# Optimization experiments

Measured on AMD Instinct MI355X. Metric: run time of the kernel, lower is better.

Reference implementation:

```python
import jax, jax.numpy as jnp
import numpy as np

D_MODEL = 2048
NUM_HEADS = 32
NUM_KV_HEADS = 8
D_K = D_MODEL // NUM_HEADS
B, S = 2, 2048


def setup_inputs() -> dict:
    key = jax.random.key(0)
    ks = jax.random.split(key, 6)
    sc = 1.0 / np.sqrt(D_MODEL)
    x = jax.random.normal(ks[0], (B, S, D_MODEL), dtype=jnp.float32)
    mask = jnp.tril(jnp.ones((S, S), dtype=jnp.float32))[None, None]  # [1,1,S,S]
    return {
        'x': x,
        'mask': mask,
        'Wq': jax.random.normal(ks[1], (D_MODEL, D_MODEL), jnp.float32) * sc,
        'bq': jnp.zeros((D_MODEL,), jnp.float32),
        'Wk': jax.random.normal(ks[2], (D_MODEL, NUM_KV_HEADS * D_K), jnp.float32) * sc,
        'bk': jnp.zeros((NUM_KV_HEADS * D_K,), jnp.float32),
        'Wv': jax.random.normal(ks[3], (D_MODEL, NUM_KV_HEADS * D_K), jnp.float32) * sc,
        'bv': jnp.zeros((NUM_KV_HEADS * D_K,), jnp.float32),
        'Wo': jax.random.normal(ks[4], (D_MODEL, D_MODEL), jnp.float32) * sc,
        'bo': jnp.zeros((D_MODEL,), jnp.float32),
    }


def reference(x, mask, Wq, bq, Wk, bk, Wv, bv, Wo, bo):
    b, s, _ = x.shape
    g = NUM_HEADS // NUM_KV_HEADS  # queries per kv head
    Q = (x @ Wq + bq).reshape(b, s, NUM_HEADS, D_K).transpose(0, 2, 1, 3)      # [b,h,s,dk]
    K = (x @ Wk + bk).reshape(b, s, NUM_KV_HEADS, D_K).transpose(0, 2, 1, 3)   # [b,kv,s,dk]
    V = (x @ Wv + bv).reshape(b, s, NUM_KV_HEADS, D_K).transpose(0, 2, 1, 3)
    # group queries per kv head instead of repeat_interleave on K/V
    Qg = Q.reshape(b, NUM_KV_HEADS, g, s, D_K)
    scores = jnp.einsum('bkgqd,bkld->bkgql', Qg, K) / np.sqrt(D_K)             # [b,kv,g,s,s]
    scores = jnp.where(mask[:, :, None] == 0, -1e9, scores)
    attn = jax.nn.softmax(scores, axis=-1)
    out = jnp.einsum('bkgql,bkld->bkgqd', attn, V)                              # [b,kv,g,s,dk]
    out = out.reshape(b, NUM_HEADS, s, D_K).transpose(0, 2, 1, 3).reshape(b, s, D_MODEL)
    return out @ Wo + bo
```

## Files before the change

kernel.cpp:

```cpp
#include <hip/hip_runtime.h>
#include <stdint.h>

typedef __bf16 bf16x8 __attribute__((ext_vector_type(8)));
typedef float  f32x4  __attribute__((ext_vector_type(4)));

__device__ __forceinline__ f32x4 mfma16(bf16x8 a, bf16x8 b, f32x4 c) {
    return __builtin_amdgcn_mfma_f32_16x16x32_bf16(a, b, c, 0, 0, 0);
}

__device__ __forceinline__ uint16_t f2bf(float f) {
    union { __bf16 b; uint16_t u; } cv; cv.b = (__bf16)f; return cv.u;
}

#if __has_builtin(__builtin_amdgcn_exp2f)
#define EXP2F(x) __builtin_amdgcn_exp2f(x)
#else
#define EXP2F(x) __expf((x) * 0.6931471805599453f)
#endif

typedef __attribute__((address_space(3))) void as3_void;
typedef __attribute__((address_space(1))) void as1_void;
__device__ __forceinline__ void async_ld16(const void* g, void* l) {
    __builtin_amdgcn_global_load_lds((const as1_void*)g, (as3_void*)l, 16, 0, 0);
}


__global__ void convert_bias(const float* __restrict__ in, uint16_t* __restrict__ out,
                             const float* __restrict__ bq, const float* __restrict__ bk,
                             const float* __restrict__ bv, float* __restrict__ biasq) {
    if (blockIdx.x < 8192) {
        int i = (blockIdx.x * 256 + threadIdx.x) * 4;
        float4 v = *(const float4*)(in + i);
        ushort4 o;
        o.x = f2bf(v.x); o.y = f2bf(v.y); o.z = f2bf(v.z); o.w = f2bf(v.w);
        *(ushort4*)(out + i) = o;
    } else {
        int i = (blockIdx.x - 8192) * 256 + threadIdx.x;
        if (i < 3072)
            biasq[i] = (i < 2048) ? bq[i] : (i < 2560 ? bk[i - 2048] : bv[i - 2560]);
    }
}

__global__ void transpose_w(const float* __restrict__ Wq, const float* __restrict__ Wk,
                            const float* __restrict__ Wv, const float* __restrict__ Wo,
                            uint16_t* __restrict__ wqkvT, uint16_t* __restrict__ woT) {
    __shared__ float tile[32][33];
    const int z = blockIdx.z;
    const float* in; uint16_t* out; int ldin, off;
    if (z == 0)      { in = Wq; out = wqkvT; ldin = 2048; off = 0; }
    else if (z == 1) { if (blockIdx.x >= 16) return; in = Wk; out = wqkvT; ldin = 512; off = 2048; }
    else if (z == 2) { if (blockIdx.x >= 16) return; in = Wv; out = wqkvT; ldin = 512; off = 2560; }
    else             { in = Wo; out = woT;   ldin = 2048; off = 0; }
    const int c0 = blockIdx.x << 5, r0 = blockIdx.y << 5;
    const int tx = threadIdx.x, ty = threadIdx.y;
#pragma unroll
    for (int i = 0; i < 4; ++i)
        tile[ty + i * 8][tx] = in[(size_t)(r0 + ty + i * 8) * ldin + c0 + tx];
    __syncthreads();
#pragma unroll
    for (int i = 0; i < 4; ++i)
        out[(size_t)(off + c0 + ty + i * 8) * 2048 + r0 + tx] = f2bf(tile[tx][ty + i * 8]);
}

__global__ void transpose_v(const uint16_t* __restrict__ qkv, uint16_t* __restrict__ vt) {
    __shared__ uint16_t tile[32][33];
    const int c0 = blockIdx.x << 5, r0 = blockIdx.y << 5, b = blockIdx.z;
    const int tx = threadIdx.x, ty = threadIdx.y;
#pragma unroll
    for (int i = 0; i < 4; ++i)
        tile[ty + i * 8][tx] = qkv[(size_t)(b * 2048 + r0 + ty + i * 8) * 3072 + 2560 + c0 + tx];
    __syncthreads();
    const int perm = 4 * (tx >> 3) + (((tx & 7) < 4) ? 0 : 16) + (tx & 3);
#pragma unroll
    for (int i = 0; i < 4; ++i)
        vt[(size_t)(b * 512 + c0 + ty + i * 8) * 2048 + r0 + tx] = tile[perm][ty + i * 8];
}

template <bool F32OUT>
__global__ __launch_bounds__(256, 2)
void gemm_bt(const uint16_t* __restrict__ A, const uint16_t* __restrict__ Bt,
             const float* __restrict__ bias, void* __restrict__ Cout, int N, int K) {
    __shared__ __align__(16) uint16_t As[8192];
    __shared__ __align__(16) uint16_t Bs[8192];
    const int tid = threadIdx.x;
    const int wv = tid >> 6, ln = tid & 63;
    const int quad = ln >> 4, l16 = ln & 15;
    const int row0 = blockIdx.y << 7, col0 = blockIdx.x << 7;
    const int wm = wv >> 1, wn = wv & 1;

    const uint16_t* gA[4];
    const uint16_t* gB[4];
#pragma unroll
    for (int j = 0; j < 4; ++j) {
        int p = j * 256 + tid;
        int r = p >> 3, c = (p & 7) ^ ((r ^ (r >> 3)) & 7);
        gA[j] = A + (size_t)(row0 + r) * K + (c << 3);
        gB[j] = Bt + (size_t)(col0 + r) * K + (c << 3);
    }

    int a_off[4][2], b_off[4][2];
#pragma unroll
    for (int t = 0; t < 4; ++t)
#pragma unroll
        for (int s = 0; s < 2; ++s) {
            int r = (wm << 6) + (t << 4) + l16;
            a_off[t][s] = (((r << 3) + ((4 * s + quad) ^ ((r ^ (r >> 3)) & 7))) << 3);
            r = (wn << 6) + (t << 4) + l16;
            b_off[t][s] = (((r << 3) + ((4 * s + quad) ^ ((r ^ (r >> 3)) & 7))) << 3);
        }

    f32x4 acc[4][4] = {};

    for (int k0 = 0; k0 < K; k0 += 64) {
        __syncthreads();
#pragma unroll
        for (int j = 0; j < 4; ++j) {
            async_ld16(gA[j] + k0, As + (j << 11) + (wv << 9));
            async_ld16(gB[j] + k0, Bs + (j << 11) + (wv << 9));
        }
        __syncthreads();
#pragma unroll
        for (int s = 0; s < 2; ++s) {
            bf16x8 af[4], bfr[4];
#pragma unroll
            for (int t = 0; t < 4; ++t) af[t] = *(const bf16x8*)(As + a_off[t][s]);
#pragma unroll
            for (int t = 0; t < 4; ++t) bfr[t] = *(const bf16x8*)(Bs + b_off[t][s]);
#pragma unroll
            for (int mt = 0; mt < 4; ++mt)
#pragma unroll
                for (int nt = 0; nt < 4; ++nt)
                    acc[mt][nt] = mfma16(af[mt], bfr[nt], acc[mt][nt]);
        }
    }

#pragma unroll
    for (int nt = 0; nt < 4; ++nt) {
        const int col = col0 + (wn << 6) + (nt << 4) + l16;
        const float bv = bias[col];
#pragma unroll
        for (int mt = 0; mt < 4; ++mt) {
            const int rbase = row0 + (wm << 6) + (mt << 4) + (quad << 2);
#pragma unroll
            for (int r = 0; r < 4; ++r) {
                float v = acc[mt][nt][r] + bv;
                if (F32OUT)
                    ((float*)Cout)[(size_t)(rbase + r) * N + col] = v;
                else
                    ((uint16_t*)Cout)[(size_t)(rbase + r) * N + col] = f2bf(v);
            }
        }
    }
}

__global__ __launch_bounds__(256, 2)
void attn_fwd(const uint16_t* __restrict__ QKV, const uint16_t* __restrict__ Vt,
              uint16_t* __restrict__ AO) {
    __shared__ __align__(16) uint16_t smem[16384];
    uint16_t* const Ks = smem;
    uint16_t* const Vs = smem + 8192;

    const int tid = threadIdx.x;
    const int wv = tid >> 6, ln = tid & 63;
    const int quad = ln >> 4, l16 = ln & 15;
    const int p = blockIdx.x, kvh = blockIdx.y, b = blockIdx.z;
    const int h = kvh * 4 + wv;

    const uint16_t* Kg = QKV + (size_t)(b * 2048) * 3072 + 2048 + kvh * 64;
    const uint16_t* Vg = Vt + (size_t)(b * 512 + kvh * 64) * 2048;

    const uint16_t* gK[2];
    const uint16_t* gV[2];
#pragma unroll
    for (int j = 0; j < 2; ++j) {
        int pos = j * 256 + tid;
        int r = pos >> 3, c = (pos & 7) ^ ((r ^ (r >> 3)) & 7);
        gK[j] = Kg + (size_t)r * 3072 + (c << 3);
        gV[j] = Vg + (size_t)r * 2048 + (c << 3);
    }
    const int sdst = wv << 9;

    int kf_off[4][2], vf_off[2][4];
#pragma unroll
    for (int g = 0; g < 4; ++g) {
        int r = g * 16 + l16, gs = (r ^ (r >> 3)) & 7;
#pragma unroll
        for (int kk = 0; kk < 2; ++kk)
            kf_off[g][kk] = ((r << 3) + ((kk * 4 + quad) ^ gs)) << 3;
    }
#pragma unroll
    for (int nt = 0; nt < 4; ++nt) {
        int r = nt * 16 + l16, gs = (r ^ (r >> 3)) & 7;
#pragma unroll
        for (int s = 0; s < 2; ++s)
            vf_off[s][nt] = ((r << 3) + ((s * 4 + quad) ^ gs)) << 3;
    }

#define EXP_PV(MASKED)                                                         \
    _Pragma("unroll")                                                          \
    for (int m = 0; m < 2; ++m) {                                              \
        f32x4 ev[4];                                                           \
        _Pragma("unroll")                                                      \
        for (int g = 0; g < 4; ++g) {                                          \
            f32x4 arg = sv[m][g] * 0.18033688f + (-23.0831207f);               \
            _Pragma("unroll")                                                  \
            for (int rr = 0; rr < 4; ++rr) {                                   \
                float v = EXP2F(arg[rr]);                                      \
                if (MASKED && (16 * g + 4 * quad + rr >                        \
                               32 * wr + 16 * m + l16)) v = 0.0f;              \
                ev[g][rr] = v;                                                 \
            }                                                                  \
        }                                                                      \
        f32x4 s2 = (ev[0] + ev[1]) + (ev[2] + ev[3]);                          \
        lp[m] += (s2[0] + s2[1]) + (s2[2] + s2[3]);                            \
        bf16x8 pf0, pf1;                                                       \
        _Pragma("unroll")                                                      \
        for (int rr = 0; rr < 4; ++rr) {                                       \
            pf0[rr] = (__bf16)ev[0][rr]; pf0[4 + rr] = (__bf16)ev[1][rr];      \
            pf1[rr] = (__bf16)ev[2][rr]; pf1[4 + rr] = (__bf16)ev[3][rr];      \
        }                                                                      \
        __builtin_amdgcn_s_setprio(1);                                         \
        _Pragma("unroll")                                                      \
        for (int nt = 0; nt < 4; ++nt) {                                       \
            acc[m][nt] = mfma16(vf[0][nt], pf0, acc[m][nt]);                   \
            acc[m][nt] = mfma16(vf[1][nt], pf1, acc[m][nt]);                   \
        }                                                                      \
        __builtin_amdgcn_s_setprio(0);                                         \
    }

#pragma unroll
    for (int half = 0; half < 2; ++half) {
        const int w = half ? (63 - p) : p;
        const int q0 = w << 5;
        const int nkb = (w >> 1) + 1;
        const int wr = w & 1;

        bf16x8 qf[2][2];
#pragma unroll
        for (int m = 0; m < 2; ++m)
#pragma unroll
            for (int kk = 0; kk < 2; ++kk)
                qf[m][kk] = *(const bf16x8*)(QKV +
                    (size_t)(b * 2048 + q0 + m * 16 + l16) * 3072 + h * 64 + kk * 32 + quad * 8);

        f32x4 acc[2][4] = {};
        float lp[2] = {0.0f, 0.0f};

        __syncthreads();
#pragma unroll
        for (int j = 0; j < 2; ++j) {
            async_ld16(gK[j], Ks + (j << 11) + sdst);
            async_ld16(gV[j], Vs + (j << 11) + sdst);
        }

        for (int t = 0; t < nkb; ++t) {
            const int cur = t & 1;
            __syncthreads();
            if (t + 1 < nkb) {
                const size_t ko = (size_t)((t + 1) << 6) * 3072;
                const int vo = (t + 1) << 6;
#pragma unroll
                for (int j = 0; j < 2; ++j) {
                    async_ld16(gK[j] + ko, Ks + ((cur ^ 1) << 12) + (j << 11) + sdst);
                    async_ld16(gV[j] + vo, Vs + ((cur ^ 1) << 12) + (j << 11) + sdst);
                }
            }

            bf16x8 kf[4][2], vf[2][4];
#pragma unroll
            for (int g = 0; g < 4; ++g)
#pragma unroll
                for (int kk = 0; kk < 2; ++kk)
                    kf[g][kk] = *(const bf16x8*)(Ks + (cur << 12) + kf_off[g][kk]);
#pragma unroll
            for (int s = 0; s < 2; ++s)
#pragma unroll
                for (int nt = 0; nt < 4; ++nt)
                    vf[s][nt] = *(const bf16x8*)(Vs + (cur << 12) + vf_off[s][nt]);

            f32x4 sv[2][4];
            __builtin_amdgcn_s_setprio(1);
#pragma unroll
            for (int m = 0; m < 2; ++m)
#pragma unroll
                for (int g = 0; g < 4; ++g) {
                    f32x4 z = {0.f, 0.f, 0.f, 0.f};
                    z = mfma16(kf[g][0], qf[m][0], z);
                    z = mfma16(kf[g][1], qf[m][1], z);
                    sv[m][g] = z;
                }
            __builtin_amdgcn_s_setprio(0);

            if (t < nkb - 1) {
                EXP_PV(false)
            } else {
                EXP_PV(true)
            }
        }

        float inv[2];
#pragma unroll
        for (int m = 0; m < 2; ++m) {
            float rs = lp[m];
            rs += __shfl_xor(rs, 16, 64);
            rs += __shfl_xor(rs, 32, 64);
            inv[m] = 1.0f / rs;
        }

        __syncthreads();
        uint16_t* ot = smem + wv * 2176;
#pragma unroll
        for (int m = 0; m < 2; ++m)
#pragma unroll
            for (int nt = 0; nt < 4; ++nt)
#pragma unroll
                for (int pp = 0; pp < 2; ++pp) {
                    uint32_t pk = (uint32_t)f2bf(acc[m][nt][2 * pp] * inv[m]) |
                                  ((uint32_t)f2bf(acc[m][nt][2 * pp + 1] * inv[m]) << 16);
                    *(uint32_t*)(ot + (m * 16 + l16) * 68 + nt * 16 + quad * 4 + 2 * pp) = pk;
                }
        const int orow = ln >> 1, ohalf = (ln & 1) << 5;
        uint16_t* aobase = AO + (size_t)(b * 2048 + q0 + orow) * 2048 + h * 64 + ohalf;
        const uint16_t* osrc = ot + orow * 68 + ohalf;
#pragma unroll
        for (int c4 = 0; c4 < 4; ++c4)
            *(uint4*)(aobase + c4 * 8) = *(const uint4*)(osrc + c4 * 8);
    }
#undef EXP_PV
}


extern "C" void kernel_launch(void* const* d_in, const int* in_sizes, int n_in,
                              void* d_out, int out_size, void* d_ws, size_t ws_size,
                              hipStream_t stream) {
    (void)in_sizes; (void)n_in; (void)out_size; (void)ws_size;
    const float* x  = (const float*)d_in[0];
    const float* Wq = (const float*)d_in[2];
    const float* bq = (const float*)d_in[3];
    const float* Wk = (const float*)d_in[4];
    const float* bk = (const float*)d_in[5];
    const float* Wv = (const float*)d_in[6];
    const float* bv = (const float*)d_in[7];
    const float* Wo = (const float*)d_in[8];
    const float* bo = (const float*)d_in[9];

    char* ws = (char*)d_ws;
    uint16_t* xb    = (uint16_t*)ws;
    uint16_t* wqkvT = (uint16_t*)(ws + 16777216);
    uint16_t* woT   = (uint16_t*)(ws + 16777216 + 12582912);
    float*    biasq = (float*)(ws + 16777216 + 12582912 + 8388608);
    uint16_t* qkv   = (uint16_t*)d_out;
    uint16_t* ao    = xb;
    uint16_t* vt    = wqkvT;

    dim3 tb(32, 8);
    convert_bias<<<8204, 256, 0, stream>>>(x, xb, bq, bk, bv, biasq);
    transpose_w<<<dim3(64, 64, 4), tb, 0, stream>>>(Wq, Wk, Wv, Wo, wqkvT, woT);
    gemm_bt<false><<<dim3(24, 32), 256, 0, stream>>>(xb, wqkvT, biasq, qkv, 3072, 2048);
    transpose_v<<<dim3(16, 64, 2), tb, 0, stream>>>(qkv, vt);
    attn_fwd<<<dim3(32, 8, 2), 256, 0, stream>>>(qkv, vt, ao);
    gemm_bt<true><<<dim3(16, 32), 256, 0, stream>>>(ao, woT, bo, d_out, 2048, 2048);
}
```

Baseline: 283.6 us.

## Merge prep kernels and double K/V tile window per attention barrier

Fuses the x-to-bf16 conversion and bias packing into the weight transpose kernel as an extra z-slice, removing one launch. In attention, each barrier iteration now prefetches and processes two 64-key K/V sub-tiles instead of one, with LDS doubled to 64 KB. This halves the number of __syncthreads per query block and gives loads more lead time, but the larger LDS footprint may limit occupancy against the two-blocks-per-CU launch bound.

```diff
diff --git a/kernel.cpp b/kernel.cpp
--- a/kernel.cpp
+++ b/kernel.cpp
@@ -25,34 +25,39 @@
 }
 
 
-__global__ void convert_bias(const float* __restrict__ in, uint16_t* __restrict__ out,
-                             const float* __restrict__ bq, const float* __restrict__ bk,
-                             const float* __restrict__ bv, float* __restrict__ biasq) {
-    if (blockIdx.x < 8192) {
-        int i = (blockIdx.x * 256 + threadIdx.x) * 4;
-        float4 v = *(const float4*)(in + i);
-        ushort4 o;
-        o.x = f2bf(v.x); o.y = f2bf(v.y); o.z = f2bf(v.z); o.w = f2bf(v.w);
-        *(ushort4*)(out + i) = o;
-    } else {
-        int i = (blockIdx.x - 8192) * 256 + threadIdx.x;
-        if (i < 3072)
-            biasq[i] = (i < 2048) ? bq[i] : (i < 2560 ? bk[i - 2048] : bv[i - 2560]);
-    }
-}
-
-__global__ void transpose_w(const float* __restrict__ Wq, const float* __restrict__ Wk,
-                            const float* __restrict__ Wv, const float* __restrict__ Wo,
-                            uint16_t* __restrict__ wqkvT, uint16_t* __restrict__ woT) {
+__global__ void prep_wx(const float* __restrict__ x,
+                        const float* __restrict__ Wq, const float* __restrict__ Wk,
+                        const float* __restrict__ Wv, const float* __restrict__ Wo,
+                        const float* __restrict__ bq, const float* __restrict__ bk,
+                        const float* __restrict__ bv,
+                        uint16_t* __restrict__ wqkvT, uint16_t* __restrict__ woT,
+                        uint16_t* __restrict__ xb, float* __restrict__ biasq) {
+    const int z = blockIdx.z;
+    const int tx = threadIdx.x, ty = threadIdx.y;
+    if (z == 4) {
+        const int tid = ty * 32 + tx;
+        const int linear = blockIdx.y * 64 + blockIdx.x;
+        const int i = linear * 2048 + tid * 8;
+#pragma unroll
+        for (int u = 0; u < 2; ++u) {
+            float4 v = *(const float4*)(x + i + u * 4);
+            ushort4 o;
+            o.x = f2bf(v.x); o.y = f2bf(v.y); o.z = f2bf(v.z); o.w = f2bf(v.w);
+            *(ushort4*)(xb + i + u * 4) = o;
+        }
+        if (linear < 12) {
+            int bi = linear * 256 + tid;
+            biasq[bi] = (bi < 2048) ? bq[bi] : (bi < 2560 ? bk[bi - 2048] : bv[bi - 2560]);
+        }
+        return;
+    }
     __shared__ float tile[32][33];
-    const int z = blockIdx.z;
     const float* in; uint16_t* out; int ldin, off;
     if (z == 0)      { in = Wq; out = wqkvT; ldin = 2048; off = 0; }
     else if (z == 1) { if (blockIdx.x >= 16) return; in = Wk; out = wqkvT; ldin = 512; off = 2048; }
     else if (z == 2) { if (blockIdx.x >= 16) return; in = Wv; out = wqkvT; ldin = 512; off = 2560; }
     else             { in = Wo; out = woT;   ldin = 2048; off = 0; }
     const int c0 = blockIdx.x << 5, r0 = blockIdx.y << 5;
-    const int tx = threadIdx.x, ty = threadIdx.y;
 #pragma unroll
     for (int i = 0; i < 4; ++i)
         tile[ty + i * 8][tx] = in[(size_t)(r0 + ty + i * 8) * ldin + c0 + tx];
@@ -156,9 +161,9 @@
 __global__ __launch_bounds__(256, 2)
 void attn_fwd(const uint16_t* __restrict__ QKV, const uint16_t* __restrict__ Vt,
               uint16_t* __restrict__ AO) {
-    __shared__ __align__(16) uint16_t smem[16384];
+    __shared__ __align__(16) uint16_t smem[32768];
     uint16_t* const Ks = smem;
-    uint16_t* const Vs = smem + 8192;
+    uint16_t* const Vs = smem + 16384;
 
     const int tid = threadIdx.x;
     const int wv = tid >> 6, ln = tid & 63;
@@ -228,11 +233,43 @@
         __builtin_amdgcn_s_setprio(0);                                         \
     }
 
+#define PROC(SUB)                                                              \
+    {                                                                          \
+        const uint16_t* kb = Ks + (((cur << 1) | SUB) << 12);                  \
+        const uint16_t* vb = Vs + (((cur << 1) | SUB) << 12);                  \
+        bf16x8 kf[4][2], vf[2][4];                                             \
+        _Pragma("unroll")                                                      \
+        for (int g = 0; g < 4; ++g)                                            \
+            _Pragma("unroll")                                                  \
+            for (int kk = 0; kk < 2; ++kk)                                     \
+                kf[g][kk] = *(const bf16x8*)(kb + kf_off[g][kk]);              \
+        _Pragma("unroll")                                                      \
+        for (int s = 0; s < 2; ++s)                                            \
+            _Pragma("unroll")                                                  \
+            for (int nt = 0; nt < 4; ++nt)                                     \
+                vf[s][nt] = *(const bf16x8*)(vb + vf_off[s][nt]);              \
+        f32x4 sv[2][4];                                                        \
+        __builtin_amdgcn_s_setprio(1);                                         \
+        _Pragma("unroll")                                                      \
+        for (int m = 0; m < 2; ++m)                                            \
+            _Pragma("unroll")                                                  \
+            for (int g = 0; g < 4; ++g) {                                      \
+                f32x4 z = {0.f, 0.f, 0.f, 0.f};                                \
+                z = mfma16(kf[g][0], qf[m][0], z);                             \
+                z = mfma16(kf[g][1], qf[m][1], z);                             \
+                sv[m][g] = z;                                                  \
+            }                                                                  \
+        __builtin_amdgcn_s_setprio(0);                                         \
+        if ((tw << 1) + SUB == nkb - 1) { EXP_PV(true) }                       \
+        else                            { EXP_PV(false) }                      \
+    }
+
 #pragma unroll
     for (int half = 0; half < 2; ++half) {
         const int w = half ? (63 - p) : p;
         const int q0 = w << 5;
         const int nkb = (w >> 1) + 1;
+        const int nwin = (nkb + 1) >> 1;
         const int wr = w & 1;
 
         bf16x8 qf[2][2];
@@ -248,54 +285,34 @@
 
         __syncthreads();
 #pragma unroll
-        for (int j = 0; j < 2; ++j) {
-            async_ld16(gK[j], Ks + (j << 11) + sdst);
-            async_ld16(gV[j], Vs + (j << 11) + sdst);
-        }
-
-        for (int t = 0; t < nkb; ++t) {
-            const int cur = t & 1;
+        for (int sub = 0; sub < 2; ++sub)
+#pragma unroll
+            for (int j = 0; j < 2; ++j) {
+                async_ld16(gK[j] + (size_t)(sub << 6) * 3072, Ks + (sub << 12) + (j << 11) + sdst);
+                async_ld16(gV[j] + (sub << 6),                Vs + (sub << 12) + (j << 11) + sdst);
+            }
+
+        for (int tw = 0; tw < nwin; ++tw) {
+            const int cur = tw & 1;
             __syncthreads();
-            if (t + 1 < nkb) {
-                const size_t ko = (size_t)((t + 1) << 6) * 3072;
-                const int vo = (t + 1) << 6;
-#pragma unroll
-                for (int j = 0; j < 2; ++j) {
-                    async_ld16(gK[j] + ko, Ks + ((cur ^ 1) << 12) + (j << 11) + sdst);
-                    async_ld16(gV[j] + vo, Vs + ((cur ^ 1) << 12) + (j << 11) + sdst);
+            if (tw + 1 < nwin) {
+#pragma unroll
+                for (int sub = 0; sub < 2; ++sub) {
+                    const int tn = ((tw + 1) << 1) + sub;
+                    const size_t ko = (size_t)(tn << 6) * 3072;
+                    const int vo = tn << 6;
+#pragma unroll
+                    for (int j = 0; j < 2; ++j) {
+                        async_ld16(gK[j] + ko,
+                                   Ks + ((((cur ^ 1) << 1) | sub) << 12) + (j << 11) + sdst);
+                        async_ld16(gV[j] + vo,
+                                   Vs + ((((cur ^ 1) << 1) | sub) << 12) + (j << 11) + sdst);
+                    }
                 }
             }
 
-            bf16x8 kf[4][2], vf[2][4];
-#pragma unroll
-            for (int g = 0; g < 4; ++g)
-#pragma unroll
-                for (int kk = 0; kk < 2; ++kk)
-                    kf[g][kk] = *(const bf16x8*)(Ks + (cur << 12) + kf_off[g][kk]);
-#pragma unroll
-            for (int s = 0; s < 2; ++s)
-#pragma unroll
-                for (int nt = 0; nt < 4; ++nt)
-                    vf[s][nt] = *(const bf16x8*)(Vs + (cur << 12) + vf_off[s][nt]);
-
-            f32x4 sv[2][4];
-            __builtin_amdgcn_s_setprio(1);
-#pragma unroll
-            for (int m = 0; m < 2; ++m)
-#pragma unroll
-                for (int g = 0; g < 4; ++g) {
-                    f32x4 z = {0.f, 0.f, 0.f, 0.f};
-                    z = mfma16(kf[g][0], qf[m][0], z);
-                    z = mfma16(kf[g][1], qf[m][1], z);
-                    sv[m][g] = z;
-                }
-            __builtin_amdgcn_s_setprio(0);
-
-            if (t < nkb - 1) {
-                EXP_PV(false)
-            } else {
-                EXP_PV(true)
-            }
+            PROC(0)
+            if ((tw << 1) + 1 < nkb) PROC(1)
         }
 
         float inv[2];
@@ -326,6 +343,7 @@
         for (int c4 = 0; c4 < 4; ++c4)
             *(uint4*)(aobase + c4 * 8) = *(const uint4*)(osrc + c4 * 8);
     }
+#undef PROC
 #undef EXP_PV
 }
 
@@ -354,8 +372,8 @@
     uint16_t* vt    = wqkvT;
 
     dim3 tb(32, 8);
-    convert_bias<<<8204, 256, 0, stream>>>(x, xb, bq, bk, bv, biasq);
-    transpose_w<<<dim3(64, 64, 4), tb, 0, stream>>>(Wq, Wk, Wv, Wo, wqkvT, woT);
+    prep_wx<<<dim3(64, 64, 5), tb, 0, stream>>>(x, Wq, Wk, Wv, Wo, bq, bk, bv,
+                                                wqkvT, woT, xb, biasq);
     gemm_bt<false><<<dim3(24, 32), 256, 0, stream>>>(xb, wqkvT, biasq, qkv, 3072, 2048);
     transpose_v<<<dim3(16, 64, 2), tb, 0, stream>>>(qkv, vt);
     attn_fwd<<<dim3(32, 8, 2), 256, 0, stream>>>(qkv, vt, ao);
```

Measured after the change: 285.6 us. No clear change (+0.7%).

## Process both causal query tiles concurrently in 512-thread attention blocks sharing K/V

Applied to the files above, without the earlier changes.

The attention kernel grows from 256 to 512 threads. The two query tiles each block handles (p and 63-p) now run at the same time in separate 4-wave groups instead of one after the other. Each K/V tile is loaded into LDS once and used by both groups, so the short-tile group simply idles once its own range is done. This halves K/V staging traffic and the serial second pass. The cost is idle waves in the short group, a larger LDS footprint for the output staging, and possible register pressure under launch_bounds(512,2).

```diff
diff --git a/kernel.cpp b/kernel.cpp
--- a/kernel.cpp
+++ b/kernel.cpp
@@ -153,10 +153,10 @@
     }
 }
 
-__global__ __launch_bounds__(256, 2)
+__global__ __launch_bounds__(512, 2)
 void attn_fwd(const uint16_t* __restrict__ QKV, const uint16_t* __restrict__ Vt,
               uint16_t* __restrict__ AO) {
-    __shared__ __align__(16) uint16_t smem[16384];
+    __shared__ __align__(16) uint16_t smem[17408];
     uint16_t* const Ks = smem;
     uint16_t* const Vs = smem + 8192;
 
@@ -164,19 +164,23 @@
     const int wv = tid >> 6, ln = tid & 63;
     const int quad = ln >> 4, l16 = ln & 15;
     const int p = blockIdx.x, kvh = blockIdx.y, b = blockIdx.z;
-    const int h = kvh * 4 + wv;
+    const int wg = wv >> 2;
+    const int h = kvh * 4 + (wv & 3);
+    const int w = wg ? (63 - p) : p;
+    const int q0 = w << 5;
+    const int nkbw = (w >> 1) + 1;
+    const int nkbm = ((63 - p) >> 1) + 1;
+    const int wr = w & 1;
 
     const uint16_t* Kg = QKV + (size_t)(b * 2048) * 3072 + 2048 + kvh * 64;
     const uint16_t* Vg = Vt + (size_t)(b * 512 + kvh * 64) * 2048;
 
-    const uint16_t* gK[2];
-    const uint16_t* gV[2];
-#pragma unroll
-    for (int j = 0; j < 2; ++j) {
-        int pos = j * 256 + tid;
-        int r = pos >> 3, c = (pos & 7) ^ ((r ^ (r >> 3)) & 7);
-        gK[j] = Kg + (size_t)r * 3072 + (c << 3);
-        gV[j] = Vg + (size_t)r * 2048 + (c << 3);
+    const uint16_t* gK;
+    const uint16_t* gV;
+    {
+        int r = tid >> 3, c = (tid & 7) ^ ((r ^ (r >> 3)) & 7);
+        gK = Kg + (size_t)r * 3072 + (c << 3);
+        gV = Vg + (size_t)r * 2048 + (c << 3);
     }
     const int sdst = wv << 9;
 
@@ -195,6 +199,17 @@
         for (int s = 0; s < 2; ++s)
             vf_off[s][nt] = ((r << 3) + ((s * 4 + quad) ^ gs)) << 3;
     }
+
+    bf16x8 qf[2][2];
+#pragma unroll
+    for (int m = 0; m < 2; ++m)
+#pragma unroll
+        for (int kk = 0; kk < 2; ++kk)
+            qf[m][kk] = *(const bf16x8*)(QKV +
+                (size_t)(b * 2048 + q0 + m * 16 + l16) * 3072 + h * 64 + kk * 32 + quad * 8);
+
+    f32x4 acc[2][4] = {};
+    float lp[2] = {0.0f, 0.0f};
 
 #define EXP_PV(MASKED)                                                         \
     _Pragma("unroll")                                                          \
@@ -228,44 +243,18 @@
         __builtin_amdgcn_s_setprio(0);                                         \
     }
 
-#pragma unroll
-    for (int half = 0; half < 2; ++half) {
-        const int w = half ? (63 - p) : p;
-        const int q0 = w << 5;
-        const int nkb = (w >> 1) + 1;
-        const int wr = w & 1;
-
-        bf16x8 qf[2][2];
-#pragma unroll
-        for (int m = 0; m < 2; ++m)
-#pragma unroll
-            for (int kk = 0; kk < 2; ++kk)
-                qf[m][kk] = *(const bf16x8*)(QKV +
-                    (size_t)(b * 2048 + q0 + m * 16 + l16) * 3072 + h * 64 + kk * 32 + quad * 8);
-
-        f32x4 acc[2][4] = {};
-        float lp[2] = {0.0f, 0.0f};
-
+    async_ld16(gK, Ks + sdst);
+    async_ld16(gV, Vs + sdst);
+
+    for (int t = 0; t < nkbm; ++t) {
+        const int cur = t & 1;
         __syncthreads();
-#pragma unroll
-        for (int j = 0; j < 2; ++j) {
-            async_ld16(gK[j], Ks + (j << 11) + sdst);
-            async_ld16(gV[j], Vs + (j << 11) + sdst);
-        }
-
-        for (int t = 0; t < nkb; ++t) {
-            const int cur = t & 1;
-            __syncthreads();
-            if (t + 1 < nkb) {
-                const size_t ko = (size_t)((t + 1) << 6) * 3072;
-                const int vo = (t + 1) << 6;
-#pragma unroll
-                for (int j = 0; j < 2; ++j) {
-                    async_ld16(gK[j] + ko, Ks + ((cur ^ 1) << 12) + (j << 11) + sdst);
-                    async_ld16(gV[j] + vo, Vs + ((cur ^ 1) << 12) + (j << 11) + sdst);
-                }
-            }
-
+        if (t + 1 < nkbm) {
+            async_ld16(gK + (size_t)((t + 1) << 6) * 3072, Ks + ((cur ^ 1) << 12) + sdst);
+            async_ld16(gV + ((t + 1) << 6),                Vs + ((cur ^ 1) << 12) + sdst);
+        }
+
+        if (t < nkbw) {
             bf16x8 kf[4][2], vf[2][4];
 #pragma unroll
             for (int g = 0; g < 4; ++g)
@@ -291,42 +280,42 @@
                 }
             __builtin_amdgcn_s_setprio(0);
 
-            if (t < nkb - 1) {
+            if (t < nkbw - 1) {
                 EXP_PV(false)
             } else {
                 EXP_PV(true)
             }
         }
-
-        float inv[2];
-#pragma unroll
-        for (int m = 0; m < 2; ++m) {
-            float rs = lp[m];
-            rs += __shfl_xor(rs, 16, 64);
-            rs += __shfl_xor(rs, 32, 64);
-            inv[m] = 1.0f / rs;
-        }
-
-        __syncthreads();
-        uint16_t* ot = smem + wv * 2176;
-#pragma unroll
-        for (int m = 0; m < 2; ++m)
-#pragma unroll
-            for (int nt = 0; nt < 4; ++nt)
-#pragma unroll
-                for (int pp = 0; pp < 2; ++pp) {
-                    uint32_t pk = (uint32_t)f2bf(acc[m][nt][2 * pp] * inv[m]) |
-                                  ((uint32_t)f2bf(acc[m][nt][2 * pp + 1] * inv[m]) << 16);
-                    *(uint32_t*)(ot + (m * 16 + l16) * 68 + nt * 16 + quad * 4 + 2 * pp) = pk;
-                }
-        const int orow = ln >> 1, ohalf = (ln & 1) << 5;
-        uint16_t* aobase = AO + (size_t)(b * 2048 + q0 + orow) * 2048 + h * 64 + ohalf;
-        const uint16_t* osrc = ot + orow * 68 + ohalf;
-#pragma unroll
-        for (int c4 = 0; c4 < 4; ++c4)
-            *(uint4*)(aobase + c4 * 8) = *(const uint4*)(osrc + c4 * 8);
     }
 #undef EXP_PV
+
+    float inv[2];
+#pragma unroll
+    for (int m = 0; m < 2; ++m) {
+        float rs = lp[m];
+        rs += __shfl_xor(rs, 16, 64);
+        rs += __shfl_xor(rs, 32, 64);
+        inv[m] = 1.0f / rs;
+    }
+
+    __syncthreads();
+    uint16_t* ot = smem + wv * 2176;
+#pragma unroll
+    for (int m = 0; m < 2; ++m)
+#pragma unroll
+        for (int nt = 0; nt < 4; ++nt)
+#pragma unroll
+            for (int pp = 0; pp < 2; ++pp) {
+                uint32_t pk = (uint32_t)f2bf(acc[m][nt][2 * pp] * inv[m]) |
+                              ((uint32_t)f2bf(acc[m][nt][2 * pp + 1] * inv[m]) << 16);
+                *(uint32_t*)(ot + (m * 16 + l16) * 68 + nt * 16 + quad * 4 + 2 * pp) = pk;
+            }
+    const int orow = ln >> 1, ohalf = (ln & 1) << 5;
+    uint16_t* aobase = AO + (size_t)(b * 2048 + q0 + orow) * 2048 + h * 64 + ohalf;
+    const uint16_t* osrc = ot + orow * 68 + ohalf;
+#pragma unroll
+    for (int c4 = 0; c4 < 4; ++c4)
+        *(uint4*)(aobase + c4 * 8) = *(const uint4*)(osrc + c4 * 8);
 }
 
 
@@ -358,6 +347,6 @@
     transpose_w<<<dim3(64, 64, 4), tb, 0, stream>>>(Wq, Wk, Wv, Wo, wqkvT, woT);
     gemm_bt<false><<<dim3(24, 32), 256, 0, stream>>>(xb, wqkvT, biasq, qkv, 3072, 2048);
     transpose_v<<<dim3(16, 64, 2), tb, 0, stream>>>(qkv, vt);
-    attn_fwd<<<dim3(32, 8, 2), 256, 0, stream>>>(qkv, vt, ao);
+    attn_fwd<<<dim3(32, 8, 2), 512, 0, stream>>>(qkv, vt, ao);
     gemm_bt<true><<<dim3(16, 32), 256, 0, stream>>>(ao, woT, bo, d_out, 2048, 2048);
 }
```

Measured after the change: 317.6 us. +12.0%, slower.

## Fuse fp32-to-bf16 conversion of x into QKV GEMM tile loads

Applied to the files above, without the earlier changes.

Drops the separate x-to-bf16 conversion kernel. The QKV GEMM now loads fp32 x tiles directly into LDS with a swizzled layout and converts them to bf16 in registers before the MFMA. The bias packing moves into an extra z-slice of the weight transpose kernel. This removes one launch and a 16MB write plus read of bf16 x. In exchange the GEMM moves twice the A-tile bytes per k-step, uses 48KB of LDS, and adds conversion ALU work, which may limit occupancy and throughput.

```diff
diff --git a/kernel.cpp b/kernel.cpp
--- a/kernel.cpp
+++ b/kernel.cpp
@@ -25,34 +25,28 @@
 }
 
 
-__global__ void convert_bias(const float* __restrict__ in, uint16_t* __restrict__ out,
-                             const float* __restrict__ bq, const float* __restrict__ bk,
-                             const float* __restrict__ bv, float* __restrict__ biasq) {
-    if (blockIdx.x < 8192) {
-        int i = (blockIdx.x * 256 + threadIdx.x) * 4;
-        float4 v = *(const float4*)(in + i);
-        ushort4 o;
-        o.x = f2bf(v.x); o.y = f2bf(v.y); o.z = f2bf(v.z); o.w = f2bf(v.w);
-        *(ushort4*)(out + i) = o;
-    } else {
-        int i = (blockIdx.x - 8192) * 256 + threadIdx.x;
-        if (i < 3072)
-            biasq[i] = (i < 2048) ? bq[i] : (i < 2560 ? bk[i - 2048] : bv[i - 2560]);
-    }
-}
-
 __global__ void transpose_w(const float* __restrict__ Wq, const float* __restrict__ Wk,
                             const float* __restrict__ Wv, const float* __restrict__ Wo,
-                            uint16_t* __restrict__ wqkvT, uint16_t* __restrict__ woT) {
+                            const float* __restrict__ bq, const float* __restrict__ bk,
+                            const float* __restrict__ bv,
+                            uint16_t* __restrict__ wqkvT, uint16_t* __restrict__ woT,
+                            float* __restrict__ biasq) {
+    const int z = blockIdx.z;
+    const int tx = threadIdx.x, ty = threadIdx.y;
+    if (z == 4) {
+        const int linear = blockIdx.y * 64 + blockIdx.x;
+        if (linear >= 12) return;
+        int bi = linear * 256 + ty * 32 + tx;
+        biasq[bi] = (bi < 2048) ? bq[bi] : (bi < 2560 ? bk[bi - 2048] : bv[bi - 2560]);
+        return;
+    }
     __shared__ float tile[32][33];
-    const int z = blockIdx.z;
     const float* in; uint16_t* out; int ldin, off;
     if (z == 0)      { in = Wq; out = wqkvT; ldin = 2048; off = 0; }
     else if (z == 1) { if (blockIdx.x >= 16) return; in = Wk; out = wqkvT; ldin = 512; off = 2048; }
     else if (z == 2) { if (blockIdx.x >= 16) return; in = Wv; out = wqkvT; ldin = 512; off = 2560; }
     else             { in = Wo; out = woT;   ldin = 2048; off = 0; }
     const int c0 = blockIdx.x << 5, r0 = blockIdx.y << 5;
-    const int tx = threadIdx.x, ty = threadIdx.y;
 #pragma unroll
     for (int i = 0; i < 4; ++i)
         tile[ty + i * 8][tx] = in[(size_t)(r0 + ty + i * 8) * ldin + c0 + tx];
@@ -76,35 +70,60 @@
         vt[(size_t)(b * 512 + c0 + ty + i * 8) * 2048 + r0 + tx] = tile[perm][ty + i * 8];
 }
 
-template <bool F32OUT>
+template <bool F32OUT, bool AF32>
 __global__ __launch_bounds__(256, 2)
-void gemm_bt(const uint16_t* __restrict__ A, const uint16_t* __restrict__ Bt,
-             const float* __restrict__ bias, void* __restrict__ Cout, int N, int K) {
-    __shared__ __align__(16) uint16_t As[8192];
-    __shared__ __align__(16) uint16_t Bs[8192];
+void gemm_bt(const uint16_t* __restrict__ A, const float* __restrict__ A32,
+             const uint16_t* __restrict__ Bt, const float* __restrict__ bias,
+             void* __restrict__ Cout, int N, int K) {
+    constexpr int ABYTES = AF32 ? 32768 : 16384;
+    __shared__ __align__(16) char smem[ABYTES + 16384];
+    uint16_t* const Bs = (uint16_t*)(smem + ABYTES);
     const int tid = threadIdx.x;
     const int wv = tid >> 6, ln = tid & 63;
     const int quad = ln >> 4, l16 = ln & 15;
     const int row0 = blockIdx.y << 7, col0 = blockIdx.x << 7;
     const int wm = wv >> 1, wn = wv & 1;
 
-    const uint16_t* gA[4];
     const uint16_t* gB[4];
 #pragma unroll
     for (int j = 0; j < 4; ++j) {
         int p = j * 256 + tid;
         int r = p >> 3, c = (p & 7) ^ ((r ^ (r >> 3)) & 7);
-        gA[j] = A + (size_t)(row0 + r) * K + (c << 3);
         gB[j] = Bt + (size_t)(col0 + r) * K + (c << 3);
     }
-
-    int a_off[4][2], b_off[4][2];
+    const uint16_t* gA[4];
+    const float* gA32[8];
+    if (AF32) {
+#pragma unroll
+        for (int j = 0; j < 8; ++j) {
+            int p = j * 256 + tid;
+            int r = p >> 4, q = p & 15, cf = q >> 1, h = q & 1;
+            int sf = ((cf ^ ((r ^ (r >> 3)) & 7)) << 3) + ((h ^ (r & 1)) << 2);
+            gA32[j] = A32 + (size_t)(row0 + r) * K + sf;
+        }
+    } else {
+#pragma unroll
+        for (int j = 0; j < 4; ++j) {
+            int p = j * 256 + tid;
+            int r = p >> 3, c = (p & 7) ^ ((r ^ (r >> 3)) & 7);
+            gA[j] = A + (size_t)(row0 + r) * K + (c << 3);
+        }
+    }
+
+    int a_lo[4][2], a_hi[4][2], b_off[4][2];
 #pragma unroll
     for (int t = 0; t < 4; ++t)
 #pragma unroll
         for (int s = 0; s < 2; ++s) {
             int r = (wm << 6) + (t << 4) + l16;
-            a_off[t][s] = (((r << 3) + ((4 * s + quad) ^ ((r ^ (r >> 3)) & 7))) << 3);
+            int gs = (r ^ (r >> 3)) & 7;
+            if (AF32) {
+                int base = (r << 4) + (((4 * s + quad) ^ gs) << 1);
+                a_lo[t][s] = (base + (r & 1)) << 4;
+                a_hi[t][s] = (base + (1 ^ (r & 1))) << 4;
+            } else {
+                a_lo[t][s] = (((r << 3) + ((4 * s + quad) ^ gs)) << 3);
+            }
             r = (wn << 6) + (t << 4) + l16;
             b_off[t][s] = (((r << 3) + ((4 * s + quad) ^ ((r ^ (r >> 3)) & 7))) << 3);
         }
@@ -113,17 +132,38 @@
 
     for (int k0 = 0; k0 < K; k0 += 64) {
         __syncthreads();
-#pragma unroll
-        for (int j = 0; j < 4; ++j) {
-            async_ld16(gA[j] + k0, As + (j << 11) + (wv << 9));
+        if (AF32) {
+#pragma unroll
+            for (int j = 0; j < 8; ++j)
+                async_ld16(gA32[j] + k0, smem + (j << 12) + (wv << 10));
+        } else {
+#pragma unroll
+            for (int j = 0; j < 4; ++j)
+                async_ld16(gA[j] + k0, (uint16_t*)smem + (j << 11) + (wv << 9));
+        }
+#pragma unroll
+        for (int j = 0; j < 4; ++j)
             async_ld16(gB[j] + k0, Bs + (j << 11) + (wv << 9));
-        }
         __syncthreads();
 #pragma unroll
         for (int s = 0; s < 2; ++s) {
             bf16x8 af[4], bfr[4];
 #pragma unroll
-            for (int t = 0; t < 4; ++t) af[t] = *(const bf16x8*)(As + a_off[t][s]);
+            for (int t = 0; t < 4; ++t) {
+                if (AF32) {
+                    f32x4 lo = *(const f32x4*)(smem + a_lo[t][s]);
+                    f32x4 hi = *(const f32x4*)(smem + a_hi[t][s]);
+                    bf16x8 a;
+#pragma unroll
+                    for (int i = 0; i < 4; ++i) {
+                        a[i] = (__bf16)lo[i];
+                        a[4 + i] = (__bf16)hi[i];
+                    }
+                    af[t] = a;
+                } else {
+                    af[t] = *(const bf16x8*)((uint16_t*)smem + a_lo[t][s]);
+                }
+            }
 #pragma unroll
             for (int t = 0; t < 4; ++t) bfr[t] = *(const bf16x8*)(Bs + b_off[t][s]);
 #pragma unroll
@@ -345,19 +385,20 @@
     const float* bo = (const float*)d_in[9];
 
     char* ws = (char*)d_ws;
-    uint16_t* xb    = (uint16_t*)ws;
+    uint16_t* ao    = (uint16_t*)ws;
     uint16_t* wqkvT = (uint16_t*)(ws + 16777216);
     uint16_t* woT   = (uint16_t*)(ws + 16777216 + 12582912);
     float*    biasq = (float*)(ws + 16777216 + 12582912 + 8388608);
     uint16_t* qkv   = (uint16_t*)d_out;
-    uint16_t* ao    = xb;
     uint16_t* vt    = wqkvT;
 
     dim3 tb(32, 8);
-    convert_bias<<<8204, 256, 0, stream>>>(x, xb, bq, bk, bv, biasq);
-    transpose_w<<<dim3(64, 64, 4), tb, 0, stream>>>(Wq, Wk, Wv, Wo, wqkvT, woT);
-    gemm_bt<false><<<dim3(24, 32), 256, 0, stream>>>(xb, wqkvT, biasq, qkv, 3072, 2048);
+    transpose_w<<<dim3(64, 64, 5), tb, 0, stream>>>(Wq, Wk, Wv, Wo, bq, bk, bv,
+                                                    wqkvT, woT, biasq);
+    gemm_bt<false, true><<<dim3(24, 32), 256, 0, stream>>>(
+        nullptr, x, wqkvT, biasq, qkv, 3072, 2048);
     transpose_v<<<dim3(16, 64, 2), tb, 0, stream>>>(qkv, vt);
     attn_fwd<<<dim3(32, 8, 2), 256, 0, stream>>>(qkv, vt, ao);
-    gemm_bt<true><<<dim3(16, 32), 256, 0, stream>>>(ao, woT, bo, d_out, 2048, 2048);
-}
+    gemm_bt<true, false><<<dim3(16, 32), 256, 0, stream>>>(
+        ao, nullptr, woT, bo, d_out, 2048, 2048);
+}
```

After: 306.4 us. +8.0%, slower.
